# Kernel optimization log

Hardware: AMD Instinct MI355X
Metric: run time of the kernel (lower is better)

Reference implementation:

```python
import jax, jax.numpy as jnp
import numpy as np
import math

B, N, D, S = 128, 2048, 512, 64  # batch, nodes, d_model, state_features


def setup_inputs() -> dict:
    key = jax.random.key(0)
    k1, k2, k3, k4, k5 = jax.random.split(key, 5)
    node_embeddings = jax.random.normal(k1, (B, N, D), dtype=jnp.float32)
    truck_state = jax.random.normal(k2, (B, S), dtype=jnp.float32)
    mask = jax.random.bernoulli(k3, 0.3, (B, N))  # True = masked-out node
    Wq = jax.random.normal(k4, (D, S), dtype=jnp.float32) * 0.05  # query_proj weight
    bq = jnp.zeros((D,), dtype=jnp.float32)
    Ws = jax.random.normal(k5, (D, D), dtype=jnp.float32) * 0.02  # scores_proj weight
    bs = jnp.zeros((D,), dtype=jnp.float32)
    return {"node_embeddings": node_embeddings, "truck_state": truck_state,
            "mask": mask, "Wq": Wq, "bq": bq, "Ws": Ws, "bs": bs}


def reference(node_embeddings, truck_state, mask, Wq, bq, Ws, bs):
    d_model = node_embeddings.shape[-1]
    scale = 1.0 / math.sqrt(d_model)
    # query = query_proj(truck_state): [B, D]
    query = truck_state @ Wq.T + bq
    # single-query attention scores over nodes: [B, N]
    attn_scores = jnp.einsum('bd,bnd->bn', query, node_embeddings) * scale
    attn_scores = jnp.where(mask, -jnp.inf, attn_scores)
    attn_weights = jax.nn.softmax(attn_scores, axis=-1)
    # context: [B, D]
    context = jnp.einsum('bn,bnd->bd', attn_weights, node_embeddings)
    # scores = scores_proj(context): [B, D]
    scores = context @ Ws.T + bs
    # dot-product logits per node: [B, N]
    logits = jnp.einsum('bnd,bd->bn', node_embeddings, scores) * scale
    logits = jnp.where(mask, -jnp.inf, logits)
    return logits
```

## Files before the change

### kernel.cpp

```cpp
#include <hip/hip_runtime.h>
#include <math.h>
#include <float.h>

#define BB 128
#define NN 2048
#define DD 512
#define SS 64
#define NCHUNK 8
#define CH (NN / NCHUNK)
#define SCALE 0.044194173824159216f
#define NEG_BIG (-1.0e30f)

__global__ __launch_bounds__(512) void k_pass1(
    const float* __restrict__ node, const unsigned char* __restrict__ mask,
    const float* __restrict__ ts, const float* __restrict__ Wq,
    const float* __restrict__ bq,
    float* __restrict__ part_ctx, float* __restrict__ part_m,
    float* __restrict__ part_l)
{
    int bc    = blockIdx.x;
    int b     = bc >> 3;
    int chunk = bc & 7;
    int wave  = threadIdx.x >> 6;
    int lane  = threadIdx.x & 63;
    int dbase = lane * 8;

    __shared__ float q_lds[DD];
    {
        int d = threadIdx.x;
        const float4* tv = (const float4*)(ts + b * SS);
        const float4* wv = (const float4*)(Wq + (size_t)d * SS);
        float acc = 0.f;
#pragma unroll
        for (int k = 0; k < SS / 4; ++k) {
            float4 a = tv[k], w = wv[k];
            acc += a.x * w.x + a.y * w.y + a.z * w.z + a.w * w.w;
        }
        q_lds[d] = acc + bq[d];
    }
    __syncthreads();

    float4 q0 = *(const float4*)&q_lds[dbase];
    float4 q1 = *(const float4*)&q_lds[dbase + 4];

    float m = NEG_BIG, l = 0.f;
    float c0 = 0, c1 = 0, c2 = 0, c3 = 0, c4 = 0, c5 = 0, c6 = 0, c7 = 0;

    const unsigned char* mrow = mask + (size_t)b * NN;
    int n0 = chunk * CH + wave * (CH / 8);

    for (int i = 0; i < CH / 8; ++i) {
        int n = n0 + i;
        if (mrow[n] != 0) continue;
        const float* row = node + ((size_t)b * NN + n) * DD + dbase;
        float4 v0 = *(const float4*)row;
        float4 v1 = *(const float4*)(row + 4);
        float dp = q0.x * v0.x + q0.y * v0.y + q0.z * v0.z + q0.w * v0.w
                 + q1.x * v1.x + q1.y * v1.y + q1.z * v1.z + q1.w * v1.w;
#pragma unroll
        for (int off = 32; off; off >>= 1) dp += __shfl_xor(dp, off, 64);
        float s  = dp * SCALE;
        float nm = fmaxf(m, s);
        float r  = __expf(m - nm);
        float p  = __expf(s - nm);
        l = l * r + p;
        c0 = c0 * r + p * v0.x; c1 = c1 * r + p * v0.y;
        c2 = c2 * r + p * v0.z; c3 = c3 * r + p * v0.w;
        c4 = c4 * r + p * v1.x; c5 = c5 * r + p * v1.y;
        c6 = c6 * r + p * v1.z; c7 = c7 * r + p * v1.w;
        m = nm;
    }

    __shared__ float lds_m[8];
    __shared__ float lds_l[8];
    __shared__ float lds_ctx[8][DD];
    if (lane == 0) { lds_m[wave] = m; lds_l[wave] = l; }
    __syncthreads();

    float M = lds_m[0];
#pragma unroll
    for (int w = 1; w < 8; ++w) M = fmaxf(M, lds_m[w]);

    float f = __expf(m - M);
    float4 s0 = make_float4(c0 * f, c1 * f, c2 * f, c3 * f);
    float4 s1 = make_float4(c4 * f, c5 * f, c6 * f, c7 * f);
    *(float4*)&lds_ctx[wave][dbase]     = s0;
    *(float4*)&lds_ctx[wave][dbase + 4] = s1;
    __syncthreads();

    int d = threadIdx.x;
    float acc = 0.f;
#pragma unroll
    for (int w = 0; w < 8; ++w) acc += lds_ctx[w][d];
    part_ctx[(size_t)bc * DD + d] = acc;

    if (threadIdx.x == 0) {
        float L = 0.f;
#pragma unroll
        for (int w = 0; w < 8; ++w) L += __expf(lds_m[w] - M) * lds_l[w];
        part_m[bc] = M;
        part_l[bc] = L;
    }
}

__global__ __launch_bounds__(256) void k_combine(
    const float* __restrict__ part_ctx, const float* __restrict__ part_m,
    const float* __restrict__ part_l,
    const float* __restrict__ Ws, const float* __restrict__ bs,
    float* __restrict__ scores)
{
    int b = blockIdx.x;
    __shared__ float ctx[DD];

    float M = NEG_BIG;
#pragma unroll
    for (int c = 0; c < NCHUNK; ++c) M = fmaxf(M, part_m[b * NCHUNK + c]);
    float f[NCHUNK];
    float L = 0.f;
#pragma unroll
    for (int c = 0; c < NCHUNK; ++c) {
        f[c] = __expf(part_m[b * NCHUNK + c] - M);
        L += f[c] * part_l[b * NCHUNK + c];
    }
    float Linv = 1.f / fmaxf(L, 1e-30f);

    for (int d = threadIdx.x; d < DD; d += 256) {
        float acc = 0.f;
#pragma unroll
        for (int c = 0; c < NCHUNK; ++c)
            acc += f[c] * part_ctx[(size_t)(b * NCHUNK + c) * DD + d];
        ctx[d] = acc * Linv;
    }
    __syncthreads();

    for (int d = threadIdx.x; d < DD; d += 256) {
        const float4* w = (const float4*)(Ws + (size_t)d * DD);
        float acc = 0.f;
#pragma unroll 8
        for (int k = 0; k < DD / 4; ++k) {
            float4 wv = w[k];
            acc += wv.x * ctx[4 * k] + wv.y * ctx[4 * k + 1]
                 + wv.z * ctx[4 * k + 2] + wv.w * ctx[4 * k + 3];
        }
        scores[b * DD + d] = acc + bs[d];
    }
}

__global__ __launch_bounds__(256) void k_logits(
    const float* __restrict__ node, const unsigned char* __restrict__ mask,
    const float* __restrict__ scores, float* __restrict__ out)
{
    int g    = blockIdx.x * 4 + (threadIdx.x >> 6);
    int lane = threadIdx.x & 63;
    int b    = g >> 11;
    if (mask[g] != 0) {
        if (lane == 0) out[g] = NEG_BIG;
        return;
    }
    int dbase = lane * 8;
    const float* row = node + (size_t)g * DD + dbase;
    float4 v0 = *(const float4*)row;
    float4 v1 = *(const float4*)(row + 4);
    const float* sc = scores + b * DD + dbase;
    float4 s0 = *(const float4*)sc;
    float4 s1 = *(const float4*)(sc + 4);
    float dp = v0.x * s0.x + v0.y * s0.y + v0.z * s0.z + v0.w * s0.w
             + v1.x * s1.x + v1.y * s1.y + v1.z * s1.z + v1.w * s1.w;
#pragma unroll
    for (int off = 32; off; off >>= 1) dp += __shfl_xor(dp, off, 64);
    if (lane == 0) out[g] = dp * SCALE;
}

extern "C" void kernel_launch(void* const* d_in, const int* in_sizes, int n_in,
                              void* d_out, int out_size, void* d_ws, size_t ws_size,
                              hipStream_t stream)
{
    const float*         node = (const float*)d_in[0];
    const float*         ts   = (const float*)d_in[1];
    const unsigned char* mask = (const unsigned char*)d_in[2];
    const float*         Wq   = (const float*)d_in[3];
    const float*         bq   = (const float*)d_in[4];
    const float*         Ws   = (const float*)d_in[5];
    const float*         bs   = (const float*)d_in[6];
    float* out = (float*)d_out;

    float* ws       = (float*)d_ws;
    float* part_ctx = ws;
    float* part_m   = part_ctx + BB * NCHUNK * DD;
    float* part_l   = part_m + BB * NCHUNK;
    float* scores   = part_l + BB * NCHUNK;

    k_pass1  <<<BB * NCHUNK, 512, 0, stream>>>(node, mask, ts, Wq, bq,
                                               part_ctx, part_m, part_l);
    k_combine<<<BB, 256, 0, stream>>>(part_ctx, part_m, part_l, Ws, bs, scores);
    k_logits <<<(BB * NN) / 4, 256, 0, stream>>>(node, mask, scores, out);
}
```

Before: 243.3 us.

## Split batch in halves so logits pass rereads node data from cache

Runs the three kernels separately for each half of the batch, so the node embeddings read by pass1 (about 256 MB per half) may still sit in the large last-level cache when the logits kernel rereads them. It also doubles the chunks per batch in pass1 to keep the grid size the same, and has each logits wave process 8 rows with the scores vector loaded once. The cost is six launches instead of three, and less parallelism in each launch of the serial combine kernel.

```diff
diff --git a/kernel.cpp b/kernel.cpp
--- a/kernel.cpp
+++ b/kernel.cpp
@@ -1,13 +1,13 @@
 #include <hip/hip_runtime.h>
 #include <math.h>
-#include <float.h>
 
 #define BB 128
 #define NN 2048
 #define DD 512
 #define SS 64
-#define NCHUNK 8
-#define CH (NN / NCHUNK)
+#define HB (BB / 2)
+#define NCH 16
+#define CH (NN / NCH)
 #define SCALE 0.044194173824159216f
 #define NEG_BIG (-1.0e30f)
 
@@ -16,14 +16,15 @@
     const float* __restrict__ ts, const float* __restrict__ Wq,
     const float* __restrict__ bq,
     float* __restrict__ part_ctx, float* __restrict__ part_m,
-    float* __restrict__ part_l)
+    float* __restrict__ part_l, int bbase)
 {
     int bc    = blockIdx.x;
-    int b     = bc >> 3;
-    int chunk = bc & 7;
+    int b     = bbase + (bc >> 4);
+    int chunk = bc & 15;
     int wave  = threadIdx.x >> 6;
     int lane  = threadIdx.x & 63;
     int dbase = lane * 8;
+    int pc    = (b << 4) | chunk;
 
     __shared__ float q_lds[DD];
     {
@@ -92,14 +93,14 @@
     float acc = 0.f;
 #pragma unroll
     for (int w = 0; w < 8; ++w) acc += lds_ctx[w][d];
-    part_ctx[(size_t)bc * DD + d] = acc;
+    part_ctx[(size_t)pc * DD + d] = acc;
 
     if (threadIdx.x == 0) {
         float L = 0.f;
 #pragma unroll
         for (int w = 0; w < 8; ++w) L += __expf(lds_m[w] - M) * lds_l[w];
-        part_m[bc] = M;
-        part_l[bc] = L;
+        part_m[pc] = M;
+        part_l[pc] = L;
     }
 }
 
@@ -107,28 +108,28 @@
     const float* __restrict__ part_ctx, const float* __restrict__ part_m,
     const float* __restrict__ part_l,
     const float* __restrict__ Ws, const float* __restrict__ bs,
-    float* __restrict__ scores)
-{
-    int b = blockIdx.x;
+    float* __restrict__ scores, int bbase)
+{
+    int b = bbase + blockIdx.x;
     __shared__ float ctx[DD];
 
     float M = NEG_BIG;
 #pragma unroll
-    for (int c = 0; c < NCHUNK; ++c) M = fmaxf(M, part_m[b * NCHUNK + c]);
-    float f[NCHUNK];
+    for (int c = 0; c < NCH; ++c) M = fmaxf(M, part_m[(b << 4) | c]);
+    float f[NCH];
     float L = 0.f;
 #pragma unroll
-    for (int c = 0; c < NCHUNK; ++c) {
-        f[c] = __expf(part_m[b * NCHUNK + c] - M);
-        L += f[c] * part_l[b * NCHUNK + c];
+    for (int c = 0; c < NCH; ++c) {
+        f[c] = __expf(part_m[(b << 4) | c] - M);
+        L += f[c] * part_l[(b << 4) | c];
     }
     float Linv = 1.f / fmaxf(L, 1e-30f);
 
     for (int d = threadIdx.x; d < DD; d += 256) {
         float acc = 0.f;
 #pragma unroll
-        for (int c = 0; c < NCHUNK; ++c)
-            acc += f[c] * part_ctx[(size_t)(b * NCHUNK + c) * DD + d];
+        for (int c = 0; c < NCH; ++c)
+            acc += f[c] * part_ctx[(size_t)((b << 4) | c) * DD + d];
         ctx[d] = acc * Linv;
     }
     __syncthreads();
@@ -148,27 +149,34 @@
 
 __global__ __launch_bounds__(256) void k_logits(
     const float* __restrict__ node, const unsigned char* __restrict__ mask,
-    const float* __restrict__ scores, float* __restrict__ out)
-{
-    int g    = blockIdx.x * 4 + (threadIdx.x >> 6);
-    int lane = threadIdx.x & 63;
-    int b    = g >> 11;
-    if (mask[g] != 0) {
-        if (lane == 0) out[g] = NEG_BIG;
-        return;
-    }
+    const float* __restrict__ scores, float* __restrict__ out, int bbase)
+{
+    int wave  = threadIdx.x >> 6;
+    int lane  = threadIdx.x & 63;
     int dbase = lane * 8;
-    const float* row = node + (size_t)g * DD + dbase;
-    float4 v0 = *(const float4*)row;
-    float4 v1 = *(const float4*)(row + 4);
+    int g0    = (bbase << 11) + blockIdx.x * 32 + wave * 8;
+
+    int b = g0 >> 11;
     const float* sc = scores + b * DD + dbase;
     float4 s0 = *(const float4*)sc;
     float4 s1 = *(const float4*)(sc + 4);
-    float dp = v0.x * s0.x + v0.y * s0.y + v0.z * s0.z + v0.w * s0.w
-             + v1.x * s1.x + v1.y * s1.y + v1.z * s1.z + v1.w * s1.w;
-#pragma unroll
-    for (int off = 32; off; off >>= 1) dp += __shfl_xor(dp, off, 64);
-    if (lane == 0) out[g] = dp * SCALE;
+
+#pragma unroll 2
+    for (int i = 0; i < 8; ++i) {
+        int g = g0 + i;
+        if (mask[g] != 0) {
+            if (lane == 0) out[g] = NEG_BIG;
+            continue;
+        }
+        const float* row = node + (size_t)g * DD + dbase;
+        float4 v0 = *(const float4*)row;
+        float4 v1 = *(const float4*)(row + 4);
+        float dp = v0.x * s0.x + v0.y * s0.y + v0.z * s0.z + v0.w * s0.w
+                 + v1.x * s1.x + v1.y * s1.y + v1.z * s1.z + v1.w * s1.w;
+#pragma unroll
+        for (int off = 32; off; off >>= 1) dp += __shfl_xor(dp, off, 64);
+        if (lane == 0) out[g] = dp * SCALE;
+    }
 }
 
 extern "C" void kernel_launch(void* const* d_in, const int* in_sizes, int n_in,
@@ -186,12 +194,16 @@
 
     float* ws       = (float*)d_ws;
     float* part_ctx = ws;
-    float* part_m   = part_ctx + BB * NCHUNK * DD;
-    float* part_l   = part_m + BB * NCHUNK;
-    float* scores   = part_l + BB * NCHUNK;
-
-    k_pass1  <<<BB * NCHUNK, 512, 0, stream>>>(node, mask, ts, Wq, bq,
-                                               part_ctx, part_m, part_l);
-    k_combine<<<BB, 256, 0, stream>>>(part_ctx, part_m, part_l, Ws, bs, scores);
-    k_logits <<<(BB * NN) / 4, 256, 0, stream>>>(node, mask, scores, out);
-}
+    float* part_m   = part_ctx + BB * NCH * DD;
+    float* part_l   = part_m + BB * NCH;
+    float* scores   = part_l + BB * NCH;
+
+    for (int h = 0; h < 2; ++h) {
+        int bbase = h * HB;
+        k_pass1  <<<HB * NCH, 512, 0, stream>>>(node, mask, ts, Wq, bq,
+                                                part_ctx, part_m, part_l, bbase);
+        k_combine<<<HB, 256, 0, stream>>>(part_ctx, part_m, part_l,
+                                          Ws, bs, scores, bbase);
+        k_logits <<<HB * NN / 32, 256, 0, stream>>>(node, mask, scores, out, bbase);
+    }
+}
```

Measured after the change: 283.2 us. +16.4%, slower.
